# Kernel optimization log

Measured on AMD Instinct MI355X. Metric: run time of the kernel, lower is better.

## Reference

```python
import jax, jax.numpy as jnp
import numpy as np

B = 32          # claims
EVI = 5         # evidences per claim
L = 130         # max_len
H = 768         # bert_hidden_dim
K = 21          # n gaussian kernels
NL = 3          # num_labels
N = B * EVI


def _kernel_mus(n):
    mu = [1.0]
    bs = 2.0 / (n - 1)
    mu.append(1.0 - bs / 2.0)
    for i in range(1, n - 1):
        mu.append(mu[i] - bs)
    return mu


def _kernel_sigmas(n):
    return [0.001] + [0.1] * (n - 1)

MU = jnp.asarray(_kernel_mus(K), jnp.float32)      # [K]
SIGMA = jnp.asarray(_kernel_sigmas(K), jnp.float32)  # [K]


def _l2norm(x):
    # F.normalize(p=2, dim=-1, eps=1e-12)
    return x / jnp.maximum(jnp.linalg.norm(x, axis=-1, keepdims=True), 1e-12)


def _kernel_pool(sim, attn_d):
    # sim: [P, Q, D] cosine sims; attn_d: [P, D] doc mask -> [P, Q, K]
    pv = jnp.exp(-0.5 * ((sim[..., None] - MU) / SIGMA) ** 2) * attn_d[:, None, :, None]
    return pv.sum(axis=2)


def setup_inputs() -> dict:
    key = jax.random.key(0)
    ks = jax.random.split(key, 10)
    def p(k, shape, s=0.02):
        return jax.random.normal(k, shape, jnp.float32) * s
    return dict(
        hiddens=jax.random.normal(ks[0], (N, L, H), jnp.float32),
        pooled=jax.random.normal(ks[1], (N, H), jnp.float32),
        msk=jnp.ones((N, L), jnp.int32),
        seg=jax.random.randint(ks[2], (N, L), 0, 2, dtype=jnp.int32),
        W_att=p(ks[3], (1, K)), b_att=jnp.zeros((1,), jnp.float32),
        W_sel=p(ks[4], (1, K)), b_sel=jnp.zeros((1,), jnp.float32),
        Wg1=p(ks[5], (128, 2 * H)), bg1=jnp.zeros((128,), jnp.float32),
        Wg2=p(ks[6], (1, 128)), bg2=jnp.zeros((1,), jnp.float32),
        Wd=p(ks[7], (NL, 2 * H)), bd=jnp.zeros((NL,), jnp.float32),
    )


def reference(hiddens, pooled, msk, seg, W_att, b_att, W_sel, b_sel,
              Wg1, bg1, Wg2, bg2, Wd, bd):
    mask_text = msk.astype(jnp.float32).at[:, 0].set(0.0)       # [N,L] zero CLS
    segf = seg.astype(jnp.float32)
    mask_claim = (1.0 - segf) * mask_text
    mask_ev = segf * mask_text

    hn = _l2norm(hiddens)                                        # [N,L,H]

    # --- evidence selection: claim-vs-evidence kernel pooling within each row ---
    sim = jnp.einsum('nqh,ndh->nqd', hn, hn)                     # [N,L,L]
    ps = _kernel_pool(sim, mask_ev)                              # [N,L,K]
    lps = jnp.log(jnp.clip(ps, 1e-10, None)) * mask_claim[:, :, None]
    lps = lps.sum(axis=1) / (mask_claim.sum(axis=1, keepdims=True) + 1e-10)  # [N,K]
    sel = lps @ W_sel.T + b_sel                                  # [N,1]
    select_prob = jax.nn.softmax(sel.reshape(B, EVI, 1), axis=1)

    hb = hiddens.reshape(B, EVI, L, H)
    hnb = hn.reshape(B, EVI, L, H)
    mb = mask_text.reshape(B, EVI, L)
    pb = pooled.reshape(B, EVI, H)

    def proj_gat(x):
        return jnp.maximum(x @ Wg1.T + bg1, 0.0) @ Wg2.T + bg2

    # --- GAT-style aggregation; only the denoised branch feeds the output ---
    de_list = []
    for i in range(EVI):
        own_n = hnb[:, i]                                        # [B,L,H]
        own_m = jnp.repeat(mb[:, i], EVI, axis=0)                # [B*EVI,L]
        sim_i = jnp.einsum('beqh,bdh->beqd', hnb, own_n).reshape(B * EVI, L, L)
        ps_i = _kernel_pool(sim_i, own_m)                        # [B*EVI,L,K]
        score = (jnp.log(jnp.clip(ps_i, 1e-10, None)) @ W_att.T + b_att)[..., 0]
        score = jnp.where(mb.reshape(B * EVI, L) > 0, score, -10000.0)
        att = jax.nn.softmax(score, axis=1).reshape(B, EVI, L, 1)
        denoise = (att * hb).sum(axis=2)                         # [B,EVI,H]
        own_inp = jnp.broadcast_to(pb[:, i:i + 1], (B, EVI, H))
        w_de = jax.nn.softmax(proj_gat(jnp.concatenate([own_inp, denoise], -1)), axis=1)
        de_list.append((denoise * w_de).sum(axis=1))             # [B,H]

    de = jnp.stack(de_list, axis=1)                              # [B,EVI,H]
    feat = jnp.concatenate([pb, de], axis=-1) @ Wd.T + bd        # [B,EVI,NL]
    class_prob = jax.nn.softmax(feat, axis=2)
    prob = (select_prob * class_prob).sum(axis=1)                # [B,NL]
    return jnp.log(prob)
```

## Files before the change

### kernel.cpp

```cpp
#include <hip/hip_runtime.h>
#include <cstdint>
#include <cstddef>

#define BB 32
#define EV 5
#define LL 130
#define HH 768
#define KK 21
#define LP 160
#define SD 136
#define SR 130
#define RS 40

typedef __attribute__((ext_vector_type(8))) __bf16 bf16x8;
typedef __attribute__((ext_vector_type(4))) float f32x4;

__device__ __forceinline__ unsigned short f2bf(float f) {
    unsigned int u = __float_as_uint(f);
    u += 0x7FFFu + ((u >> 16) & 1u);
    return (unsigned short)(u >> 16);
}
__device__ __forceinline__ float bf2f(unsigned int s) {
    return __uint_as_float(s << 16);
}

__global__ __launch_bounds__(256) void k_prologue(const float* __restrict__ hid,
        unsigned short* __restrict__ hnbf, const float* __restrict__ wg1,
        unsigned short* __restrict__ wg1b, const float* __restrict__ pooled,
        unsigned short* __restrict__ xg, float* __restrict__ cg) {
    int bid = blockIdx.x, tid = threadIdx.x;
    if (bid < 5200) {
        int wave = tid >> 6, lane = tid & 63;
        int r = bid * 4 + wave;
        if (r >= 160 * LL) return;
        const float4* s4 = (const float4*)(hid + (size_t)r * HH);
        float4 v0 = s4[lane], v1 = s4[lane + 64], v2 = s4[lane + 128];
        float ss = v0.x*v0.x + v0.y*v0.y + v0.z*v0.z + v0.w*v0.w
                 + v1.x*v1.x + v1.y*v1.y + v1.z*v1.z + v1.w*v1.w
                 + v2.x*v2.x + v2.y*v2.y + v2.z*v2.z + v2.w*v2.w;
        #pragma unroll
        for (int m = 1; m < 64; m <<= 1) ss += __shfl_xor(ss, m, 64);
        float sc = 1.0f / fmaxf(sqrtf(ss), 1e-12f);
        ushort4 o0, o1, o2;
        o0.x = f2bf(v0.x*sc); o0.y = f2bf(v0.y*sc); o0.z = f2bf(v0.z*sc); o0.w = f2bf(v0.w*sc);
        o1.x = f2bf(v1.x*sc); o1.y = f2bf(v1.y*sc); o1.z = f2bf(v1.z*sc); o1.w = f2bf(v1.w*sc);
        o2.x = f2bf(v2.x*sc); o2.y = f2bf(v2.y*sc); o2.z = f2bf(v2.z*sc); o2.w = f2bf(v2.w*sc);
        ushort4* d4 = (ushort4*)(hnbf + (size_t)r * HH);
        d4[lane] = o0; d4[lane + 64] = o1; d4[lane + 128] = o2;
    } else if (bid < 5968) {
        int idx = (bid - 5200) * 256 + tid;
        wg1b[idx] = f2bf(wg1[idx]);
    } else if (bid < 6768) {
        int row = bid - 5968;
        int bi = row / 5;
        const float* src = pooled + (size_t)bi * HH;
        unsigned short* dst = xg + (size_t)row * 1536;
        #pragma unroll
        for (int j = 0; j < 3; j++) { int h = tid + j * 256; dst[h] = f2bf(src[h]); }
    } else {
        int slot = (bid - 6768) * 256 + tid;
        float4 z = (float4){0.f, 0.f, 0.f, 0.f};
        *(float4*)&cg[(size_t)slot * 4] = z;
    }
}

__global__ __launch_bounds__(256) void k_sim_gemm(const unsigned short* __restrict__ hnbf,
                                                  unsigned short* __restrict__ Sg) {
    int w = blockIdx.x;
    int xcd = w & 7, slot = w >> 3;
    int b = xcd * 4 + (slot / 25);
    int ei = slot % 25;
    int e = ei / 5, i = ei % 5;
    int pair = b * 25 + ei;
    const unsigned short* A = hnbf + (size_t)(b * 5 + e) * LL * HH;
    const unsigned short* B = hnbf + (size_t)(b * 5 + i) * LL * HH;
    __shared__ unsigned short As[160 * RS];
    __shared__ unsigned short Bs[160 * RS];
    int tid = threadIdx.x, lane = tid & 63, wave = tid >> 6;
    int quad = lane >> 4, l16 = lane & 15;
    int wm = (wave & 1) * 5, wn = (wave >> 1) * 5;
    f32x4 acc[5][5];
    #pragma unroll
    for (int mt = 0; mt < 5; mt++)
        #pragma unroll
        for (int nt = 0; nt < 5; nt++) acc[mt][nt] = (f32x4){0.f, 0.f, 0.f, 0.f};

    int grow[3], lslt[3];
    #pragma unroll
    for (int it = 0; it < 3; it++) {
        int s = tid + it * 256;
        int r = s >> 2;
        int rs = (r < LL) ? r : 0;
        grow[it] = rs * HH + (s & 3) * 8;
        lslt[it] = r * RS + (s & 3) * 8;
    }

    for (int k0 = 0; k0 < HH; k0 += 32) {
        #pragma unroll
        for (int it = 0; it < 3; ++it) {
            int s = tid + it * 256;
            if (s < 640) {
                *(uint4*)&As[lslt[it]] = *(const uint4*)(A + grow[it] + k0);
                *(uint4*)&Bs[lslt[it]] = *(const uint4*)(B + grow[it] + k0);
            }
        }
        __syncthreads();
        bf16x8 af[5], bfr[5];
        #pragma unroll
        for (int t = 0; t < 5; t++) {
            af[t]  = *(const bf16x8*)&As[((wm + t) * 16 + l16) * RS + quad * 8];
            bfr[t] = *(const bf16x8*)&Bs[((wn + t) * 16 + l16) * RS + quad * 8];
        }
        #pragma unroll
        for (int mt = 0; mt < 5; mt++)
            #pragma unroll
            for (int nt = 0; nt < 5; nt++)
                acc[mt][nt] = __builtin_amdgcn_mfma_f32_16x16x32_bf16(af[mt], bfr[nt], acc[mt][nt], 0, 0, 0);
        __syncthreads();
    }

    size_t base = (size_t)pair * SR * SD;
    #pragma unroll
    for (int mt = 0; mt < 5; mt++)
        #pragma unroll
        for (int nt = 0; nt < 5; nt++) {
            int R0 = (wm + mt) * 16 + quad * 4;
            int C = (wn + nt) * 16 + l16;
            if (C < SD) {
                #pragma unroll
                for (int reg = 0; reg < 4; reg++) {
                    int R = R0 + reg;
                    if (R < SR) Sg[base + (size_t)R * SD + C] = f2bf(acc[mt][nt][reg]);
                }
            }
        }
}

template <bool DIAG>
__device__ __forceinline__ void pool_body(
    int pair, int row, int lane8, bool live, int ne, int c,
    const unsigned short* __restrict__ Sg,
    const float* __restrict__ batt,
    float* __restrict__ score, float* __restrict__ selp, float* __restrict__ denp,
    const float* wdA, const float* wdE, const float* wqC,
    const float* WaL, const float* WsL, const float* CkL,
    float* redsel, float* redden) {

    const float LOG2E = 1.4426950408889634f;
    const float CA = -50.0f * LOG2E;
    const float CB = 95.0f * LOG2E;
    const float CR = -10.0f * LOG2E;
    const float C0 = -500000.0f * LOG2E;
    int tid = threadIdx.x;

    float a0[KK], a2[KK];
    #pragma unroll
    for (int k = 0; k < KK; k++) { a0[k] = 0.0f; a2[k] = 0.0f; }

    auto proc = [&](float s, int d) {
        float w = wdA[d];
        float w2 = DIAG ? wdE[d] : 0.0f;
        float pe = exp2f(fmaf(CB, s, CA * s * s));
        float rr = exp2f(CR * s);
        float sm1 = s - 1.0f;
        float e0 = exp2f(C0 * (sm1 * sm1));
        a0[0] = fmaf(w, e0, a0[0]);
        if (DIAG) a2[0] = fmaf(w2, e0, a2[0]);
        float p = pe;
        #pragma unroll
        for (int k = 1; k < KK; k++) {
            a0[k] = fmaf(w, p, a0[k]);
            if (DIAG) a2[k] = fmaf(w2, p, a2[k]);
            p *= rr;
        }
    };

    if (live) {
        const unsigned short* Srow = Sg + (size_t)pair * SR * SD + (size_t)row * SD;
        #pragma unroll
        for (int j = 0; j < 2; j++) {
            uint4 v = *(const uint4*)(Srow + lane8 * 8 + j * 64);
            int d0 = lane8 * 8 + j * 64;
            proc(bf2f(v.x & 0xFFFFu), d0 + 0); proc(bf2f(v.x >> 16), d0 + 1);
            proc(bf2f(v.y & 0xFFFFu), d0 + 2); proc(bf2f(v.y >> 16), d0 + 3);
            proc(bf2f(v.z & 0xFFFFu), d0 + 4); proc(bf2f(v.z >> 16), d0 + 5);
            proc(bf2f(v.w & 0xFFFFu), d0 + 6); proc(bf2f(v.w >> 16), d0 + 7);
        }
        proc(bf2f((unsigned int)Srow[128 + lane8]), 128 + lane8);
    }
    #pragma unroll
    for (int k = 0; k < KK; k++) {
        a0[k] += __shfl_xor(a0[k], 1, 64);
        a0[k] += __shfl_xor(a0[k], 2, 64);
        a0[k] += __shfl_xor(a0[k], 4, 64);
        if (DIAG) {
            a2[k] += __shfl_xor(a2[k], 1, 64);
            a2[k] += __shfl_xor(a2[k], 2, 64);
            a2[k] += __shfl_xor(a2[k], 4, 64);
        }
    }
    float selv = 0.0f, denv = 0.0f;
    if (live && lane8 == 0) {
        float sc = batt[0];
        #pragma unroll
        for (int k = 0; k < KK; k++)
            sc += WaL[k] * __logf(fmaxf(CkL[k] * a0[k], 1e-10f));
        score[(size_t)pair * LP + row] = sc;
        if (DIAG) {
            float cq = 0.0f;
            #pragma unroll
            for (int k = 0; k < KK; k++)
                cq += WsL[k] * __logf(fmaxf(CkL[k] * a2[k], 1e-10f));
            selv = wqC[row] * cq;
            denv = wqC[row];
        }
    }
    if (DIAG) {
        #pragma unroll
        for (int m = 8; m < 64; m <<= 1) {
            selv += __shfl_xor(selv, m, 64);
            denv += __shfl_xor(denv, m, 64);
        }
        int wave = tid >> 6, lane = tid & 63;
        if (lane == 0) { redsel[wave] = selv; redden[wave] = denv; }
        __syncthreads();
        if (tid == 0) {
            selp[ne * 5 + c] = redsel[0] + redsel[1] + redsel[2] + redsel[3];
            denp[ne * 5 + c] = redden[0] + redden[1] + redden[2] + redden[3];
        }
    }
}

__global__ __launch_bounds__(256) void k_pool(const unsigned short* __restrict__ Sg,
        const int* __restrict__ msk, const int* __restrict__ seg,
        const float* __restrict__ Watt, const float* __restrict__ batt,
        const float* __restrict__ Wsel,
        float* __restrict__ score, float* __restrict__ selp, float* __restrict__ denp) {
    __shared__ float wdA[SD], wdE[SD], wqC[SD];
    __shared__ float WaL[KK], WsL[KK], CkL[KK];
    __shared__ float redsel[4], redden[4];
    int w = blockIdx.x;
    int xcd = w & 7, slot = w >> 3;
    int b = xcd * 4 + (slot / 125);
    int rem = slot % 125;
    int ei = rem / 5, c = rem % 5;
    int e = ei / 5, i = ei % 5;
    int pair = b * 25 + ei;
    int ne = b * 5 + e, ni = b * 5 + i;
    int tid = threadIdx.x;

    if (tid < SD) {
        int d = tid;
        wdA[d] = (d >= 1 && d < LL) ? (float)msk[ni * LL + d] : 0.0f;
        float mtE = (d >= 1 && d < LL) ? (float)msk[ne * LL + d] : 0.0f;
        float sgE = (d < LL) ? (float)seg[ne * LL + d] : 0.0f;
        wdE[d] = sgE * mtE;
        wqC[d] = (1.0f - sgE) * mtE;
    }
    if (tid < KK) {
        const float LOG2E = 1.4426950408889634f;
        WaL[tid] = Watt[tid];
        WsL[tid] = Wsel[tid];
        float mu = 0.95f - 0.1f * (tid - 1);
        CkL[tid] = (tid == 0) ? 1.0f : exp2f(-50.0f * LOG2E * mu * mu);
    }
    __syncthreads();

    int row = c * 26 + (tid >> 3);
    int lane8 = tid & 7;
    bool live = (tid < 208);

    if (e == i)
        pool_body<true>(pair, row, lane8, live, ne, c, Sg, batt, score, selp, denp,
                        wdA, wdE, wqC, WaL, WsL, CkL, redsel, redden);
    else
        pool_body<false>(pair, row, lane8, live, ne, c, Sg, batt, score, selp, denp,
                         wdA, wdE, wqC, WaL, WsL, CkL, redsel, redden);
}

__global__ __launch_bounds__(256) void k_attden(const float* __restrict__ score,
        const int* __restrict__ msk, const float* __restrict__ hid,
        float* __restrict__ dn, unsigned short* __restrict__ xg) {
    int bid = blockIdx.x;
    int be = bid / 3, j = bid % 3;
    int b = be / 5, e = be % 5;
    int tid = threadIdx.x, lane = tid & 63, wave = tid >> 6;
    __shared__ float attl[5 * 132];

    for (int i = wave; i < 5; i += 4) {
        const float* srow = score + ((size_t)(b * 5 + i) * 5 + e) * LP;
        float v0, v1, v2 = -1e30f;
        {
            int q = lane;
            bool mt = (q >= 1 && msk[be * LL + q] != 0);
            v0 = mt ? srow[q] : -1e4f;
        }
        {
            int q = lane + 64;
            bool mt = (msk[be * LL + q] != 0);
            v1 = mt ? srow[q] : -1e4f;
        }
        if (lane < 2) {
            int q = lane + 128;
            bool mt = (msk[be * LL + q] != 0);
            v2 = mt ? srow[q] : -1e4f;
        }
        float mx = fmaxf(v0, fmaxf(v1, v2));
        #pragma unroll
        for (int m = 1; m < 64; m <<= 1) mx = fmaxf(mx, __shfl_xor(mx, m, 64));
        float e0 = __expf(v0 - mx), e1 = __expf(v1 - mx);
        float e2 = (lane < 2) ? __expf(v2 - mx) : 0.0f;
        float Z = e0 + e1 + e2;
        #pragma unroll
        for (int m = 1; m < 64; m <<= 1) Z += __shfl_xor(Z, m, 64);
        float iz = 1.0f / Z;
        attl[i * 132 + lane] = e0 * iz;
        attl[i * 132 + lane + 64] = e1 * iz;
        if (lane < 2) attl[i * 132 + lane + 128] = e2 * iz;
    }
    __syncthreads();

    int h = j * 256 + tid;
    float accA[5] = {0.f, 0.f, 0.f, 0.f, 0.f};
    float accB[5] = {0.f, 0.f, 0.f, 0.f, 0.f};
    const float* hb = hid + (size_t)be * LL * HH + h;
    int q = 0;
    #pragma unroll 2
    for (; q + 4 <= LL; q += 4) {
        float h0 = hb[(size_t)(q + 0) * HH];
        float h1 = hb[(size_t)(q + 1) * HH];
        float h2 = hb[(size_t)(q + 2) * HH];
        float h3 = hb[(size_t)(q + 3) * HH];
        #pragma unroll
        for (int i = 0; i < 5; i++) {
            accA[i] = fmaf(attl[i * 132 + q], h0, accA[i]);
            accB[i] = fmaf(attl[i * 132 + q + 1], h1, accB[i]);
            accA[i] = fmaf(attl[i * 132 + q + 2], h2, accA[i]);
            accB[i] = fmaf(attl[i * 132 + q + 3], h3, accB[i]);
        }
    }
    for (; q < LL; q++) {
        float hv = hb[(size_t)q * HH];
        #pragma unroll
        for (int i = 0; i < 5; i++) accA[i] = fmaf(attl[i * 132 + q], hv, accA[i]);
    }
    #pragma unroll
    for (int i = 0; i < 5; i++) {
        float v = accA[i] + accB[i];
        dn[((size_t)be * 5 + i) * HH + h] = v;
        xg[((size_t)(b * 5 + i) * 5 + e) * 1536 + HH + h] = f2bf(v);
    }
}

__global__ __launch_bounds__(256) void k_gate_gemm(const unsigned short* __restrict__ xg,
        const unsigned short* __restrict__ wg1b, float* __restrict__ cg) {
    int bid = blockIdx.x;
    int rb = bid / 3, ks = bid % 3;
    int m0 = rb * 16;
    __shared__ unsigned short As[16 * 32];
    __shared__ unsigned short Bs[128 * 32];
    int tid = threadIdx.x, lane = tid & 63, wave = tid >> 6;
    int quad = lane >> 4, l16 = lane & 15;
    f32x4 acc[2];
    acc[0] = (f32x4){0.f, 0.f, 0.f, 0.f};
    acc[1] = (f32x4){0.f, 0.f, 0.f, 0.f};

    for (int t = 0; t < 16; t++) {
        int k0 = ks * 512 + t * 32;
        if (tid < 64) {
            int row = tid >> 2, sg = tid & 3;
            *(uint4*)&As[tid * 8] = *(const uint4*)(xg + (size_t)(m0 + row) * 1536 + k0 + sg * 8);
        }
        #pragma unroll
        for (int it = 0; it < 2; it++) {
            int s = tid + it * 256;
            int row = s >> 2, sg = s & 3;
            *(uint4*)&Bs[s * 8] = *(const uint4*)(wg1b + (size_t)row * 1536 + k0 + sg * 8);
        }
        __syncthreads();
        bf16x8 af = *(const bf16x8*)&As[l16 * 32 + quad * 8];
        #pragma unroll
        for (int nt = 0; nt < 2; nt++) {
            int ct = wave * 2 + nt;
            bf16x8 bfr = *(const bf16x8*)&Bs[(ct * 16 + l16) * 32 + quad * 8];
            acc[nt] = __builtin_amdgcn_mfma_f32_16x16x32_bf16(af, bfr, acc[nt], 0, 0, 0);
        }
        __syncthreads();
    }
    #pragma unroll
    for (int nt = 0; nt < 2; nt++) {
        int C = (wave * 2 + nt) * 16 + l16;
        #pragma unroll
        for (int reg = 0; reg < 4; reg++) {
            int R = m0 + quad * 4 + reg;
            atomicAdd(&cg[(size_t)R * 128 + C], acc[nt][reg]);
        }
    }
}

__global__ __launch_bounds__(256) void k_gate_epi(const float* __restrict__ cg,
        const float* __restrict__ bg1, const float* __restrict__ wg2,
        const float* __restrict__ bg2, const float* __restrict__ dn,
        const float* __restrict__ pooled, const float* __restrict__ wd,
        const float* __restrict__ bd, float* __restrict__ feat) {
    int bi = blockIdx.x;
    int b = bi / 5, ii = bi % 5;
    __shared__ float red4[4];
    __shared__ float gL[5];
    __shared__ float deL[HH];
    int tid = threadIdx.x, lane = tid & 63, wave = tid >> 6;

    for (int e = 0; e < 5; e++) {
        float v = 0.0f;
        if (tid < 128) {
            float ccv = cg[(size_t)(bi * 5 + e) * 128 + tid] + bg1[tid];
            v = wg2[tid] * fmaxf(ccv, 0.0f);
        }
        #pragma unroll
        for (int m = 1; m < 64; m <<= 1) v += __shfl_xor(v, m, 64);
        if (lane == 0) red4[wave] = v;
        __syncthreads();
        if (tid == 0) gL[e] = red4[0] + red4[1] + bg2[0];
        __syncthreads();
    }
    float mx = gL[0];
    #pragma unroll
    for (int e = 1; e < 5; e++) mx = fmaxf(mx, gL[e]);
    float wde[5]; float z = 0.0f;
    #pragma unroll
    for (int e = 0; e < 5; e++) { wde[e] = __expf(gL[e] - mx); z += wde[e]; }
    float iz = 1.0f / z;
    #pragma unroll
    for (int e = 0; e < 5; e++) wde[e] *= iz;

    #pragma unroll
    for (int j = 0; j < 3; j++) {
        int h = tid + j * 256;
        float v = 0.0f;
        #pragma unroll
        for (int e = 0; e < 5; e++)
            v += wde[e] * dn[((size_t)(b * 5 + e) * 5 + ii) * HH + h];
        deL[h] = v;
    }
    __syncthreads();

    float part[3] = {0.0f, 0.0f, 0.0f};
    #pragma unroll
    for (int mm = 0; mm < 6; mm++) {
        int h = tid + mm * 256;
        float x = (mm < 3) ? pooled[(size_t)bi * HH + h] : deL[h - HH];
        #pragma unroll
        for (int c = 0; c < 3; c++) part[c] = fmaf(x, wd[(size_t)c * 1536 + h], part[c]);
    }
    #pragma unroll
    for (int c = 0; c < 3; c++) {
        float v = part[c];
        #pragma unroll
        for (int m = 1; m < 64; m <<= 1) v += __shfl_xor(v, m, 64);
        if (lane == 0) red4[wave] = v;
        __syncthreads();
        if (tid == 0) feat[bi * 3 + c] = red4[0] + red4[1] + red4[2] + red4[3] + bd[c];
        __syncthreads();
    }
}

__global__ __launch_bounds__(64) void k_final(const float* __restrict__ selp,
        const float* __restrict__ denp, const float* __restrict__ bsel,
        const float* __restrict__ feat, float* __restrict__ out) {
    int b = threadIdx.x;
    if (b >= BB) return;
    float sv[5]; float m = -1e30f;
    #pragma unroll
    for (int i = 0; i < 5; i++) {
        float num = 0.0f, den = 0.0f;
        #pragma unroll
        for (int c = 0; c < 5; c++) {
            num += selp[(b * 5 + i) * 5 + c];
            den += denp[(b * 5 + i) * 5 + c];
        }
        sv[i] = bsel[0] + num / (den + 1e-10f);
        m = fmaxf(m, sv[i]);
    }
    float z = 0.0f;
    #pragma unroll
    for (int i = 0; i < 5; i++) { sv[i] = __expf(sv[i] - m); z += sv[i]; }
    #pragma unroll
    for (int i = 0; i < 5; i++) sv[i] /= z;
    float prob[3] = {0.0f, 0.0f, 0.0f};
    #pragma unroll
    for (int i = 0; i < 5; i++) {
        float f0 = feat[(b * 5 + i) * 3 + 0];
        float f1 = feat[(b * 5 + i) * 3 + 1];
        float f2 = feat[(b * 5 + i) * 3 + 2];
        float mm = fmaxf(f0, fmaxf(f1, f2));
        float e0 = __expf(f0 - mm), e1 = __expf(f1 - mm), e2 = __expf(f2 - mm);
        float zz = e0 + e1 + e2;
        prob[0] += sv[i] * e0 / zz;
        prob[1] += sv[i] * e1 / zz;
        prob[2] += sv[i] * e2 / zz;
    }
    #pragma unroll
    for (int c = 0; c < 3; c++) out[b * 3 + c] = __logf(prob[c]);
}

extern "C" void kernel_launch(void* const* d_in, const int* in_sizes, int n_in,
                              void* d_out, int out_size, void* d_ws, size_t ws_size,
                              hipStream_t stream) {
    const float* hiddens = (const float*)d_in[0];
    const float* pooled  = (const float*)d_in[1];
    const int*   msk     = (const int*)d_in[2];
    const int*   seg     = (const int*)d_in[3];
    const float* Watt    = (const float*)d_in[4];
    const float* batt    = (const float*)d_in[5];
    const float* Wsel    = (const float*)d_in[6];
    const float* bsel    = (const float*)d_in[7];
    const float* Wg1     = (const float*)d_in[8];
    const float* bg1     = (const float*)d_in[9];
    const float* Wg2     = (const float*)d_in[10];
    const float* bg2     = (const float*)d_in[11];
    const float* Wd      = (const float*)d_in[12];
    const float* bd      = (const float*)d_in[13];

    char* ws = (char*)d_ws;
    size_t off = 0;
    auto alloc = [&](size_t bytes) -> void* {
        void* p = ws + off;
        off += (bytes + 255) & ~(size_t)255;
        return p;
    };
    unsigned short* hnbf   = (unsigned short*)alloc((size_t)160 * LL * HH * 2);
    unsigned short* Sg     = (unsigned short*)alloc((size_t)800 * SR * SD * 2);
    float*          score  = (float*)alloc((size_t)800 * LP * 4);
    float*          selp   = (float*)alloc((size_t)160 * 5 * 4);
    float*          denp   = (float*)alloc((size_t)160 * 5 * 4);
    float*          dn     = (float*)alloc((size_t)160 * 5 * HH * 4);
    unsigned short* xg     = (unsigned short*)alloc((size_t)800 * 1536 * 2);
    unsigned short* wg1b   = (unsigned short*)alloc((size_t)128 * 1536 * 2);
    float*          cg     = (float*)alloc((size_t)800 * 128 * 4);
    float*          feat   = (float*)alloc((size_t)800 * 3 * 4);
    (void)ws_size; (void)in_sizes; (void)n_in; (void)out_size;

    k_prologue<<<dim3(6868), dim3(256), 0, stream>>>(hiddens, hnbf, Wg1, wg1b, pooled, xg, cg);
    k_sim_gemm<<<dim3(800), dim3(256), 0, stream>>>(hnbf, Sg);
    k_pool<<<dim3(4000), dim3(256), 0, stream>>>(Sg, msk, seg, Watt, batt, Wsel, score, selp, denp);
    k_attden<<<dim3(480), dim3(256), 0, stream>>>(score, msk, hiddens, dn, xg);
    k_gate_gemm<<<dim3(150), dim3(256), 0, stream>>>(xg, wg1b, cg);
    k_gate_epi<<<dim3(160), dim3(256), 0, stream>>>(cg, bg1, Wg2, bg2, dn, pooled, Wd, bd, feat);
    k_final<<<dim3(1), dim3(64), 0, stream>>>(selp, denp, bsel, feat, (float*)d_out);
}
```

Baseline: 267.2 us.

## Double-buffer LDS tiles with register prefetch and XOR swizzle in sim GEMM

Restructures the similarity GEMM's k-loop so the next 32-wide K slice is prefetched into registers while MFMAs run on the current LDS buffer, then written into the alternate buffer. This leaves one barrier per iteration instead of two. The padded LDS rows (stride 40) are replaced by an XOR-swizzled 32-wide layout to avoid bank conflicts without padding. The cost is twice the LDS footprint and extra registers held for the prefetch, which could reduce occupancy.

```diff
diff --git a/kernel.cpp b/kernel.cpp
--- a/kernel.cpp
+++ b/kernel.cpp
@@ -10,7 +10,6 @@
 #define LP 160
 #define SD 136
 #define SR 130
-#define RS 40
 
 typedef __attribute__((ext_vector_type(8))) __bf16 bf16x8;
 typedef __attribute__((ext_vector_type(4))) float f32x4;
@@ -74,48 +73,75 @@
     int pair = b * 25 + ei;
     const unsigned short* A = hnbf + (size_t)(b * 5 + e) * LL * HH;
     const unsigned short* B = hnbf + (size_t)(b * 5 + i) * LL * HH;
-    __shared__ unsigned short As[160 * RS];
-    __shared__ unsigned short Bs[160 * RS];
+    __shared__ unsigned short As[2][160 * 32];
+    __shared__ unsigned short Bs[2][160 * 32];
     int tid = threadIdx.x, lane = tid & 63, wave = tid >> 6;
     int quad = lane >> 4, l16 = lane & 15;
     int wm = (wave & 1) * 5, wn = (wave >> 1) * 5;
-    f32x4 acc[5][5];
-    #pragma unroll
-    for (int mt = 0; mt < 5; mt++)
-        #pragma unroll
-        for (int nt = 0; nt < 5; nt++) acc[mt][nt] = (f32x4){0.f, 0.f, 0.f, 0.f};
-
-    int grow[3], lslt[3];
+
+    int goff[3];
     #pragma unroll
     for (int it = 0; it < 3; it++) {
         int s = tid + it * 256;
         int r = s >> 2;
         int rs = (r < LL) ? r : 0;
-        grow[it] = rs * HH + (s & 3) * 8;
-        lslt[it] = r * RS + (s & 3) * 8;
-    }
-
-    for (int k0 = 0; k0 < HH; k0 += 32) {
-        #pragma unroll
-        for (int it = 0; it < 3; ++it) {
+        goff[it] = rs * HH + (((s & 3) ^ ((r >> 1) & 3)) * 8);
+    }
+    int rdA[5], rdB[5];
+    #pragma unroll
+    for (int t = 0; t < 5; t++) {
+        int ra = (wm + t) * 16 + l16;
+        int rb = (wn + t) * 16 + l16;
+        rdA[t] = ra * 32 + (quad ^ ((ra >> 1) & 3)) * 8;
+        rdB[t] = rb * 32 + (quad ^ ((rb >> 1) & 3)) * 8;
+    }
+
+    uint4 rga[3], rgb[3];
+    auto LOADK = [&](int k0) {
+        #pragma unroll
+        for (int it = 0; it < 3; it++) {
             int s = tid + it * 256;
             if (s < 640) {
-                *(uint4*)&As[lslt[it]] = *(const uint4*)(A + grow[it] + k0);
-                *(uint4*)&Bs[lslt[it]] = *(const uint4*)(B + grow[it] + k0);
+                rga[it] = *(const uint4*)(A + goff[it] + k0);
+                rgb[it] = *(const uint4*)(B + goff[it] + k0);
             }
         }
-        __syncthreads();
+    };
+    auto STOREB = [&](int buf) {
+        #pragma unroll
+        for (int it = 0; it < 3; it++) {
+            int s = tid + it * 256;
+            if (s < 640) {
+                *(uint4*)&As[buf][s * 8] = rga[it];
+                *(uint4*)&Bs[buf][s * 8] = rgb[it];
+            }
+        }
+    };
+
+    f32x4 acc[5][5];
+    #pragma unroll
+    for (int mt = 0; mt < 5; mt++)
+        #pragma unroll
+        for (int nt = 0; nt < 5; nt++) acc[mt][nt] = (f32x4){0.f, 0.f, 0.f, 0.f};
+
+    LOADK(0);
+    STOREB(0);
+    __syncthreads();
+    for (int ks = 0; ks < 24; ks++) {
+        int cur = ks & 1;
+        if (ks < 23) LOADK((ks + 1) * 32);
         bf16x8 af[5], bfr[5];
         #pragma unroll
         for (int t = 0; t < 5; t++) {
-            af[t]  = *(const bf16x8*)&As[((wm + t) * 16 + l16) * RS + quad * 8];
-            bfr[t] = *(const bf16x8*)&Bs[((wn + t) * 16 + l16) * RS + quad * 8];
+            af[t]  = *(const bf16x8*)&As[cur][rdA[t]];
+            bfr[t] = *(const bf16x8*)&Bs[cur][rdB[t]];
         }
         #pragma unroll
         for (int mt = 0; mt < 5; mt++)
             #pragma unroll
             for (int nt = 0; nt < 5; nt++)
                 acc[mt][nt] = __builtin_amdgcn_mfma_f32_16x16x32_bf16(af[mt], bfr[nt], acc[mt][nt], 0, 0, 0);
+        if (ks < 23) STOREB(cur ^ 1);
         __syncthreads();
     }
 
```

After: 343.3 us. 1.29x slower.
